# Kernel tuning notes

Measured on AMD Instinct MI355X. Metric: run time of the kernel, lower is better.

Reference implementation:

```python
import jax, jax.numpy as jnp
import numpy as np

DIM = 1024
HEADS = 16
DIM_HEAD = 64
INNER = HEADS * DIM_HEAD  # 1024
SCALE = DIM_HEAD ** -0.5


def setup_inputs() -> dict:
    key = jax.random.key(0)
    k_x, k_qkv, k_ow, k_ob = jax.random.split(key, 4)
    B, N = 4, 2048
    x = jax.random.normal(k_x, (B, N, DIM), dtype=jnp.float32)
    # nn.Linear weights stored as [out, in] in torch; keep [in, out] for x @ W.
    w_qkv = jax.random.normal(k_qkv, (DIM, 3 * INNER), dtype=jnp.float32) * (DIM ** -0.5)
    w_out = jax.random.normal(k_ow, (INNER, DIM), dtype=jnp.float32) * (INNER ** -0.5)
    b_out = jax.random.normal(k_ob, (DIM,), dtype=jnp.float32) * 0.01
    return {"x": x, "w_qkv": w_qkv, "w_out": w_out, "b_out": b_out}


def reference(x, w_qkv, w_out, b_out):
    B, N, _ = x.shape
    qkv = x @ w_qkv  # [B, N, 3*inner]
    q, k, v = jnp.split(qkv, 3, axis=-1)
    # [B, N, inner] -> [B, H, N, dh]
    def to_heads(t):
        return t.reshape(B, N, HEADS, DIM_HEAD).transpose(0, 2, 1, 3)
    q, k, v = to_heads(q), to_heads(k), to_heads(v)
    attn = jnp.einsum("bhqd,bhkd->bhqk", q, k) * SCALE  # [B, H, N, N]
    attn = jax.nn.softmax(attn, axis=-1)
    out = jnp.einsum("bhqk,bhkd->bhqd", attn, v)  # [B, H, N, dh]
    out = out.transpose(0, 2, 1, 3).reshape(B, N, INNER)
    return out @ w_out + b_out
```

## Files before the change

kernel.cpp:

```cpp
#include <hip/hip_runtime.h>
#include <hip/hip_bf16.h>
#include <stdint.h>

typedef __attribute__((ext_vector_type(4))) float f32x4;
typedef __attribute__((ext_vector_type(16))) float f32x16;
typedef __attribute__((ext_vector_type(8))) short s16x8;
typedef __attribute__((ext_vector_type(4))) short s16x4;
typedef __attribute__((ext_vector_type(4))) unsigned int u32x4;

#define DEV static __device__ __forceinline__

constexpr int B_ = 4, H_ = 16, N_ = 2048;
constexpr float CL_ = 0.18033688011112042f;

DEV short f2bf(float x) {
  __hip_bfloat16 h = __float2bfloat16(x);
  return *reinterpret_cast<short*>(&h);
}

DEV uint32_t cvtpk(float lo, float hi) {
  uint32_t r;
  asm("v_cvt_pk_bf16_f32 %0, %1, %2" : "=v"(r) : "v"(lo), "v"(hi));
  return r;
}

DEV void gload16(const void* g, void* l) {
  __builtin_amdgcn_global_load_lds((const __attribute__((address_space(1))) void*)g,
                                   (__attribute__((address_space(3))) void*)l, 16, 0, 0);
}

__global__ void k_cvt(const float* __restrict__ x, short* __restrict__ xb) {
  int i = (blockIdx.x * 256 + threadIdx.x) * 8;
  const float4* p = reinterpret_cast<const float4*>(x + i);
  float4 a = p[0], b = p[1];
  s16x8 o;
  o[0] = f2bf(a.x); o[1] = f2bf(a.y); o[2] = f2bf(a.z); o[3] = f2bf(a.w);
  o[4] = f2bf(b.x); o[5] = f2bf(b.y); o[6] = f2bf(b.z); o[7] = f2bf(b.w);
  *reinterpret_cast<s16x8*>(xb + i) = o;
}

__global__ void k_tw(const float* __restrict__ W, short* __restrict__ WT, int R, int C) {
  __shared__ short t[64][72];
  int r0 = blockIdx.y * 64, c0 = blockIdx.x * 64;
  int tid = threadIdx.x;
  int r = tid >> 2, cp = (tid & 3) * 16;
  const float4* s4 = reinterpret_cast<const float4*>(W + (size_t)(r0 + r) * C + c0 + cp);
  float4 f0 = s4[0], f1 = s4[1], f2 = s4[2], f3 = s4[3];
  short* tr = &t[r][cp];
  tr[0] = f2bf(f0.x); tr[1] = f2bf(f0.y); tr[2]  = f2bf(f0.z); tr[3]  = f2bf(f0.w);
  tr[4] = f2bf(f1.x); tr[5] = f2bf(f1.y); tr[6]  = f2bf(f1.z); tr[7]  = f2bf(f1.w);
  tr[8] = f2bf(f2.x); tr[9] = f2bf(f2.y); tr[10] = f2bf(f2.z); tr[11] = f2bf(f2.w);
  tr[12] = f2bf(f3.x); tr[13] = f2bf(f3.y); tr[14] = f2bf(f3.z); tr[15] = f2bf(f3.w);
  __syncthreads();
  int cc = tid >> 2, rp = (tid & 3) * 16;
  short buf[16];
#pragma unroll
  for (int i = 0; i < 16; ++i) buf[i] = t[rp + i][cc];
  short* dst = WT + (size_t)(c0 + cc) * R + r0 + rp;
  *reinterpret_cast<s16x8*>(dst) = *reinterpret_cast<s16x8*>(buf);
  *reinterpret_cast<s16x8*>(dst + 8) = *reinterpret_cast<s16x8*>(buf + 8);
}

__global__ void k_tv(const short* __restrict__ v, short* __restrict__ vT) {
  __shared__ short t[64][72];
  int bh = blockIdx.y, n0 = blockIdx.x * 64;
  int tid = threadIdx.x;
  int r = tid >> 2, cp = (tid & 3) * 16;
  const short* src = v + ((size_t)bh * N_ + n0 + r) * 64 + cp;
  *reinterpret_cast<s16x8*>(&t[r][cp]) = *reinterpret_cast<const s16x8*>(src);
  *reinterpret_cast<s16x8*>(&t[r][cp + 8]) = *reinterpret_cast<const s16x8*>(src + 8);
  __syncthreads();
  int d = tid >> 2, np = (tid & 3) * 16;
  short buf[16];
#pragma unroll
  for (int i = 0; i < 16; ++i) buf[i] = t[np + i][d];
  short* dst = vT + ((size_t)bh * 64 + d) * N_ + n0 + np;
  *reinterpret_cast<s16x8*>(dst) = *reinterpret_cast<s16x8*>(buf);
  *reinterpret_cast<s16x8*>(dst + 8) = *reinterpret_cast<s16x8*>(buf + 8);
}

template <int EPI>
__global__ __launch_bounds__(256, 2)
void k_gemm(const short* __restrict__ A, const short* __restrict__ BT,
            int M, int N, int K,
            short* __restrict__ oq, short* __restrict__ ok, short* __restrict__ ov,
            const float* __restrict__ bias, float* __restrict__ out) {
  __shared__ short As[128 * 32];
  __shared__ short Bs[128 * 32];
  const int tid = threadIdx.x;
  const int m0 = blockIdx.x * 128, n0 = blockIdx.y * 128;
  const int lane = tid & 63, w = tid >> 6, g = lane >> 4, c = lane & 15;
  const int wr = w >> 1, wc = w & 1;
  f32x4 acc[4][4] = {};
  const int trow = tid >> 2, tk = (tid & 3) * 8;
  const short* ga = A + (size_t)(m0 + trow) * K + tk;
  const short* gb = BT + (size_t)(n0 + trow) * K + tk;
  short* la = As + tid * 8;
  short* lb = Bs + tid * 8;
  for (int k0 = 0; k0 < K; k0 += 32) {
    gload16(ga + k0, la);
    gload16(ga + (size_t)64 * K + k0, la + 2048);
    gload16(gb + k0, lb);
    gload16(gb + (size_t)64 * K + k0, lb + 2048);
    __syncthreads();
    s16x8 af[4], bf[4];
#pragma unroll
    for (int i = 0; i < 4; ++i)
      af[i] = *reinterpret_cast<const s16x8*>(As + (wr * 64 + i * 16 + c) * 32 + g * 8);
#pragma unroll
    for (int j = 0; j < 4; ++j)
      bf[j] = *reinterpret_cast<const s16x8*>(Bs + (wc * 64 + j * 16 + c) * 32 + g * 8);
#pragma unroll
    for (int i = 0; i < 4; ++i)
#pragma unroll
      for (int j = 0; j < 4; ++j)
        acc[i][j] = __builtin_amdgcn_mfma_f32_16x16x32_bf16(af[i], bf[j], acc[i][j], 0, 0, 0);
    __syncthreads();
  }
  if (EPI == 0) {
#pragma unroll
    for (int bj = 0; bj < 4; ++bj) {
      int ncol = n0 + wc * 64 + bj * 16 + c;
      int part = ncol >> 10;
      int c10 = ncol & 1023;
      int h = c10 >> 6, d = c10 & 63;
      short* dst0 = part == 0 ? oq : (part == 1 ? ok : ov);
      float qs = (part == 0) ? CL_ : 1.0f;
#pragma unroll
      for (int ai = 0; ai < 4; ++ai) {
#pragma unroll
        for (int r = 0; r < 4; ++r) {
          int mrow = m0 + wr * 64 + ai * 16 + g * 4 + r;
          int b = mrow >> 11, nr = mrow & 2047;
          dst0[((size_t)((b * H_ + h) * N_ + nr) << 6) + d] = f2bf(acc[ai][bj][r] * qs);
        }
      }
    }
  } else {
#pragma unroll
    for (int bj = 0; bj < 4; ++bj) {
      int ncol = n0 + wc * 64 + bj * 16 + c;
      float bb = bias[ncol];
#pragma unroll
      for (int ai = 0; ai < 4; ++ai) {
#pragma unroll
        for (int r = 0; r < 4; ++r) {
          int mrow = m0 + wr * 64 + ai * 16 + g * 4 + r;
          out[(size_t)mrow * N + ncol] = acc[ai][bj][r] + bb;
        }
      }
    }
  }
}

__global__ __launch_bounds__(256, 2)
void k_attn(const short* __restrict__ q, const short* __restrict__ kk,
            const short* __restrict__ vT, short* __restrict__ ao) {
  __shared__ __align__(16) char smem[65536];
  constexpr int NT = N_ / 64;
  int bh = blockIdx.x, qb = blockIdx.y;
  int b = bh >> 4, head = bh & 15;
  int tid = threadIdx.x, w = tid >> 6, lane = tid & 63;
  int half = lane >> 5, qc = lane & 31;
  const size_t ho = (size_t)bh * (N_ * 64);
  const short* Q = q + ho;
  const char* Kc = reinterpret_cast<const char*>(kk + ho);
  const char* Vc = reinterpret_cast<const char*>(vT + ho);
  int q0w = qb * 256 + w * 64;
  s16x8 qf[2][4];
#pragma unroll
  for (int i = 0; i < 2; ++i)
#pragma unroll
    for (int ks = 0; ks < 4; ++ks)
      qf[i][ks] = *reinterpret_cast<const s16x8*>(Q + (size_t)(q0w + i * 32 + qc) * 64 + ks * 16 + half * 8);
  f32x16 ot[2][2] = {};
  float lp[2] = {0.f, 0.f};
  const int rsw = (qc & 7) << 4;
  const int s_i0 = tid, s_i1 = tid + 256;
  const int s_r0 = s_i0 >> 3, s_c0 = ((s_i0 & 7) << 4) ^ ((s_r0 & 7) << 4);
  const int s_r1 = s_i1 >> 3, s_c1 = ((s_i1 & 7) << 4) ^ ((s_r1 & 7) << 4);
#define STAGE(T)                                                                       \
  {                                                                                    \
    char* nb = smem + ((T) & 3) * 16384;                                               \
    gload16(Kc + (size_t)((T) * 64 + s_r0) * 128 + s_c0, nb + s_i0 * 16);              \
    gload16(Kc + (size_t)((T) * 64 + s_r1) * 128 + s_c1, nb + s_i1 * 16);              \
    gload16(Vc + (size_t)s_r0 * 4096 + (T) * 128 + s_c0, nb + 8192 + s_i0 * 16);       \
    gload16(Vc + (size_t)s_r1 * 4096 + (T) * 128 + s_c1, nb + 8192 + s_i1 * 16);       \
  }
  STAGE(0);
  STAGE(1);
  for (int tt = 0; tt < NT; ++tt) {
    if (tt + 2 < NT) STAGE(tt + 2);
    if (tt + 2 < NT) {
      asm volatile("s_waitcnt vmcnt(8)" ::: "memory");
    } else if (tt + 1 < NT) {
      asm volatile("s_waitcnt vmcnt(4)" ::: "memory");
    } else {
      asm volatile("s_waitcnt vmcnt(0)" ::: "memory");
    }
    __builtin_amdgcn_s_barrier();
    __builtin_amdgcn_sched_barrier(0);
    const char* kb_ = smem + (tt & 3) * 16384;
    const char* vb_ = kb_ + 8192;
    s16x8 kf[2][4];
#pragma unroll
    for (int j = 0; j < 2; ++j)
#pragma unroll
      for (int ks = 0; ks < 4; ++ks)
        kf[j][ks] = *reinterpret_cast<const s16x8*>(kb_ + (j * 32 + qc) * 128 + ((ks * 32 + half * 16) ^ rsw));
    f32x16 st[2][2] = {};
    __builtin_amdgcn_s_setprio(1);
#pragma unroll
    for (int j = 0; j < 2; ++j)
#pragma unroll
      for (int i = 0; i < 2; ++i)
#pragma unroll
        for (int ks = 0; ks < 4; ++ks)
          st[j][i] = __builtin_amdgcn_mfma_f32_32x32x16_bf16(kf[j][ks], qf[i][ks], st[j][i], 0, 0, 0);
    __builtin_amdgcn_s_setprio(0);
#pragma unroll
    for (int j = 0; j < 2; ++j)
#pragma unroll
      for (int i = 0; i < 2; ++i)
#pragma unroll
        for (int r = 0; r < 16; ++r) {
          float p = __builtin_amdgcn_exp2f(st[j][i][r]);
          st[j][i][r] = p;
          lp[i] += p;
        }
    u32x4 pwv[2][4];
#pragma unroll
    for (int j = 0; j < 2; ++j)
#pragma unroll
      for (int i = 0; i < 2; ++i)
#pragma unroll
        for (int bb = 0; bb < 2; ++bb)
#pragma unroll
          for (int p = 0; p < 2; ++p) {
            uint32_t Aw = cvtpk(st[j][i][8 * bb + 2 * p], st[j][i][8 * bb + 2 * p + 1]);
            uint32_t Bw = cvtpk(st[j][i][8 * bb + 4 + 2 * p], st[j][i][8 * bb + 4 + 2 * p + 1]);
            asm volatile("v_permlane32_swap_b32 %0, %1" : "+v"(Aw), "+v"(Bw));
            pwv[i][j * 2 + bb][p] = Aw;
            pwv[i][j * 2 + bb][p + 2] = Bw;
          }
    s16x8 vf[2][4];
#pragma unroll
    for (int db = 0; db < 2; ++db)
#pragma unroll
      for (int kb4 = 0; kb4 < 4; ++kb4)
        vf[db][kb4] = *reinterpret_cast<const s16x8*>(vb_ + (db * 32 + qc) * 128 + ((kb4 * 32 + half * 16) ^ rsw));
    __builtin_amdgcn_s_setprio(1);
#pragma unroll
    for (int db = 0; db < 2; ++db)
#pragma unroll
      for (int i = 0; i < 2; ++i)
#pragma unroll
        for (int kb4 = 0; kb4 < 4; ++kb4)
          ot[db][i] = __builtin_amdgcn_mfma_f32_32x32x16_bf16(
              vf[db][kb4], __builtin_bit_cast(s16x8, pwv[i][kb4]), ot[db][i], 0, 0, 0);
    __builtin_amdgcn_s_setprio(0);
  }
#undef STAGE
  float inv[2];
#pragma unroll
  for (int i = 0; i < 2; ++i) {
    float t = lp[i] + __shfl_xor(lp[i], 32, 64);
    inv[i] = 1.f / t;
  }
  short* Oq = reinterpret_cast<short*>(smem) + w * 2304;
#pragma unroll
  for (int i = 0; i < 2; ++i) {
#pragma unroll
    for (int db = 0; db < 2; ++db)
#pragma unroll
      for (int m = 0; m < 4; ++m) {
        uint2 pk;
        pk.x = cvtpk(ot[db][i][4 * m] * inv[i], ot[db][i][4 * m + 1] * inv[i]);
        pk.y = cvtpk(ot[db][i][4 * m + 2] * inv[i], ot[db][i][4 * m + 3] * inv[i]);
        *reinterpret_cast<uint2*>(Oq + qc * 72 + db * 32 + m * 8 + half * 4) = pk;
      }
    int q2 = lane >> 1, dcol = (lane & 1) * 32;
    size_t ro = (size_t)(b * N_ + q0w + i * 32 + q2) * 1024 + head * 64 + dcol;
#pragma unroll
    for (int ch = 0; ch < 4; ++ch) {
      s16x8 vv = *reinterpret_cast<const s16x8*>(Oq + q2 * 72 + dcol + ch * 8);
      *reinterpret_cast<s16x8*>(ao + ro + ch * 8) = vv;
    }
  }
}

extern "C" void kernel_launch(void* const* d_in, const int* in_sizes, int n_in,
                              void* d_out, int out_size, void* d_ws, size_t ws_size,
                              hipStream_t stream) {
  const float* x = (const float*)d_in[0];
  const float* w_qkv = (const float*)d_in[1];
  const float* w_out = (const float*)d_in[2];
  const float* b_out = (const float*)d_in[3];
  float* out = (float*)d_out;
  char* ws = (char*)d_ws;
  short* xb    = (short*)(ws);
  short* wqkvT = (short*)(ws + 16777216);
  short* woutT = (short*)(ws + 23068672);
  short* qB    = (short*)(ws + 25165824);
  short* kB    = (short*)(ws + 41943040);
  short* vtmp  = (short*)(ws + 58720256);
  short* vTT   = (short*)(ws + 75497472);
  short* ao    = xb;

  k_cvt<<<4096, 256, 0, stream>>>(x, xb);
  k_tw<<<dim3(48, 16), 256, 0, stream>>>(w_qkv, wqkvT, 1024, 3072);
  k_tw<<<dim3(16, 16), 256, 0, stream>>>(w_out, woutT, 1024, 1024);
  k_gemm<0><<<dim3(64, 24), 256, 0, stream>>>(xb, wqkvT, 8192, 3072, 1024,
                                              qB, kB, vtmp, nullptr, nullptr);
  k_tv<<<dim3(32, 64), 256, 0, stream>>>(vtmp, vTT);
  k_attn<<<dim3(64, 8), 256, 0, stream>>>(qB, kB, vTT, ao);
  k_gemm<1><<<dim3(64, 8), 256, 0, stream>>>(ao, woutT, 8192, 1024, 1024,
                                             nullptr, nullptr, nullptr, b_out, out);
}
```

Before: 191.8 us.

## Halve attention query tile per block and double-buffer smem for higher occupancy

The attention kernel now gives each wave 32 query rows instead of 64, which doubles the grid to 1024 blocks. Shared memory drops to 32KB with two K/V stages instead of four, and launch bounds go from 2 to 4 blocks per CU. The explicit vmcnt-based prefetch of two tiles ahead becomes a one-ahead prefetch with __syncthreads at each step. The goal is higher occupancy and fewer registers per thread, at the cost of reloading K/V from global memory twice as often per query and using shallower pipelining.

```diff
diff --git a/kernel.cpp b/kernel.cpp
--- a/kernel.cpp
+++ b/kernel.cpp
@@ -153,10 +153,10 @@
   }
 }
 
-__global__ __launch_bounds__(256, 2)
+__global__ __launch_bounds__(256, 4)
 void k_attn(const short* __restrict__ q, const short* __restrict__ kk,
             const short* __restrict__ vT, short* __restrict__ ao) {
-  __shared__ __align__(16) char smem[65536];
+  __shared__ __align__(16) char smem[32768];
   constexpr int NT = N_ / 64;
   int bh = blockIdx.x, qb = blockIdx.y;
   int b = bh >> 4, head = bh & 15;
@@ -166,126 +166,102 @@
   const short* Q = q + ho;
   const char* Kc = reinterpret_cast<const char*>(kk + ho);
   const char* Vc = reinterpret_cast<const char*>(vT + ho);
-  int q0w = qb * 256 + w * 64;
-  s16x8 qf[2][4];
-#pragma unroll
-  for (int i = 0; i < 2; ++i)
-#pragma unroll
-    for (int ks = 0; ks < 4; ++ks)
-      qf[i][ks] = *reinterpret_cast<const s16x8*>(Q + (size_t)(q0w + i * 32 + qc) * 64 + ks * 16 + half * 8);
-  f32x16 ot[2][2] = {};
-  float lp[2] = {0.f, 0.f};
+  int q0w = qb * 128 + w * 32;
+  s16x8 qf[4];
+#pragma unroll
+  for (int ks = 0; ks < 4; ++ks)
+    qf[ks] = *reinterpret_cast<const s16x8*>(Q + (size_t)(q0w + qc) * 64 + ks * 16 + half * 8);
+  f32x16 ot[2] = {};
+  float lp = 0.f;
   const int rsw = (qc & 7) << 4;
   const int s_i0 = tid, s_i1 = tid + 256;
   const int s_r0 = s_i0 >> 3, s_c0 = ((s_i0 & 7) << 4) ^ ((s_r0 & 7) << 4);
   const int s_r1 = s_i1 >> 3, s_c1 = ((s_i1 & 7) << 4) ^ ((s_r1 & 7) << 4);
 #define STAGE(T)                                                                       \
   {                                                                                    \
-    char* nb = smem + ((T) & 3) * 16384;                                               \
+    char* nb = smem + ((T) & 1) * 16384;                                               \
     gload16(Kc + (size_t)((T) * 64 + s_r0) * 128 + s_c0, nb + s_i0 * 16);              \
     gload16(Kc + (size_t)((T) * 64 + s_r1) * 128 + s_c1, nb + s_i1 * 16);              \
     gload16(Vc + (size_t)s_r0 * 4096 + (T) * 128 + s_c0, nb + 8192 + s_i0 * 16);       \
     gload16(Vc + (size_t)s_r1 * 4096 + (T) * 128 + s_c1, nb + 8192 + s_i1 * 16);       \
   }
   STAGE(0);
-  STAGE(1);
+  __syncthreads();
   for (int tt = 0; tt < NT; ++tt) {
-    if (tt + 2 < NT) STAGE(tt + 2);
-    if (tt + 2 < NT) {
-      asm volatile("s_waitcnt vmcnt(8)" ::: "memory");
-    } else if (tt + 1 < NT) {
-      asm volatile("s_waitcnt vmcnt(4)" ::: "memory");
-    } else {
-      asm volatile("s_waitcnt vmcnt(0)" ::: "memory");
-    }
-    __builtin_amdgcn_s_barrier();
-    __builtin_amdgcn_sched_barrier(0);
-    const char* kb_ = smem + (tt & 3) * 16384;
+    if (tt + 1 < NT) STAGE(tt + 1);
+    const char* kb_ = smem + (tt & 1) * 16384;
     const char* vb_ = kb_ + 8192;
-    s16x8 kf[2][4];
+    f32x16 st[2];
+#pragma unroll
+    for (int j = 0; j < 2; ++j) {
+      s16x8 kfj[4];
+#pragma unroll
+      for (int ks = 0; ks < 4; ++ks)
+        kfj[ks] = *reinterpret_cast<const s16x8*>(kb_ + (j * 32 + qc) * 128 + ((ks * 32 + half * 16) ^ rsw));
+      f32x16 acc = {};
+      __builtin_amdgcn_s_setprio(1);
+#pragma unroll
+      for (int ks = 0; ks < 4; ++ks)
+        acc = __builtin_amdgcn_mfma_f32_32x32x16_bf16(kfj[ks], qf[ks], acc, 0, 0, 0);
+      __builtin_amdgcn_s_setprio(0);
+      st[j] = acc;
+    }
 #pragma unroll
     for (int j = 0; j < 2; ++j)
 #pragma unroll
-      for (int ks = 0; ks < 4; ++ks)
-        kf[j][ks] = *reinterpret_cast<const s16x8*>(kb_ + (j * 32 + qc) * 128 + ((ks * 32 + half * 16) ^ rsw));
-    f32x16 st[2][2] = {};
-    __builtin_amdgcn_s_setprio(1);
+      for (int r = 0; r < 16; ++r) {
+        float p = __builtin_amdgcn_exp2f(st[j][r]);
+        st[j][r] = p;
+        lp += p;
+      }
+    u32x4 pwv[4];
 #pragma unroll
     for (int j = 0; j < 2; ++j)
 #pragma unroll
-      for (int i = 0; i < 2; ++i)
-#pragma unroll
-        for (int ks = 0; ks < 4; ++ks)
-          st[j][i] = __builtin_amdgcn_mfma_f32_32x32x16_bf16(kf[j][ks], qf[i][ks], st[j][i], 0, 0, 0);
-    __builtin_amdgcn_s_setprio(0);
-#pragma unroll
-    for (int j = 0; j < 2; ++j)
-#pragma unroll
-      for (int i = 0; i < 2; ++i)
-#pragma unroll
-        for (int r = 0; r < 16; ++r) {
-          float p = __builtin_amdgcn_exp2f(st[j][i][r]);
-          st[j][i][r] = p;
-          lp[i] += p;
+      for (int bb = 0; bb < 2; ++bb)
+#pragma unroll
+        for (int p = 0; p < 2; ++p) {
+          uint32_t Aw = cvtpk(st[j][8 * bb + 2 * p], st[j][8 * bb + 2 * p + 1]);
+          uint32_t Bw = cvtpk(st[j][8 * bb + 4 + 2 * p], st[j][8 * bb + 4 + 2 * p + 1]);
+          asm volatile("v_permlane32_swap_b32 %0, %1" : "+v"(Aw), "+v"(Bw));
+          pwv[j * 2 + bb][p] = Aw;
+          pwv[j * 2 + bb][p + 2] = Bw;
         }
-    u32x4 pwv[2][4];
-#pragma unroll
-    for (int j = 0; j < 2; ++j)
-#pragma unroll
-      for (int i = 0; i < 2; ++i)
-#pragma unroll
-        for (int bb = 0; bb < 2; ++bb)
-#pragma unroll
-          for (int p = 0; p < 2; ++p) {
-            uint32_t Aw = cvtpk(st[j][i][8 * bb + 2 * p], st[j][i][8 * bb + 2 * p + 1]);
-            uint32_t Bw = cvtpk(st[j][i][8 * bb + 4 + 2 * p], st[j][i][8 * bb + 4 + 2 * p + 1]);
-            asm volatile("v_permlane32_swap_b32 %0, %1" : "+v"(Aw), "+v"(Bw));
-            pwv[i][j * 2 + bb][p] = Aw;
-            pwv[i][j * 2 + bb][p + 2] = Bw;
-          }
-    s16x8 vf[2][4];
-#pragma unroll
-    for (int db = 0; db < 2; ++db)
+#pragma unroll
+    for (int db = 0; db < 2; ++db) {
+      s16x8 vf[4];
 #pragma unroll
       for (int kb4 = 0; kb4 < 4; ++kb4)
-        vf[db][kb4] = *reinterpret_cast<const s16x8*>(vb_ + (db * 32 + qc) * 128 + ((kb4 * 32 + half * 16) ^ rsw));
-    __builtin_amdgcn_s_setprio(1);
-#pragma unroll
-    for (int db = 0; db < 2; ++db)
-#pragma unroll
-      for (int i = 0; i < 2; ++i)
-#pragma unroll
-        for (int kb4 = 0; kb4 < 4; ++kb4)
-          ot[db][i] = __builtin_amdgcn_mfma_f32_32x32x16_bf16(
-              vf[db][kb4], __builtin_bit_cast(s16x8, pwv[i][kb4]), ot[db][i], 0, 0, 0);
-    __builtin_amdgcn_s_setprio(0);
+        vf[kb4] = *reinterpret_cast<const s16x8*>(vb_ + (db * 32 + qc) * 128 + ((kb4 * 32 + half * 16) ^ rsw));
+      f32x16 acc = ot[db];
+      __builtin_amdgcn_s_setprio(1);
+#pragma unroll
+      for (int kb4 = 0; kb4 < 4; ++kb4)
+        acc = __builtin_amdgcn_mfma_f32_32x32x16_bf16(
+            vf[kb4], __builtin_bit_cast(s16x8, pwv[kb4]), acc, 0, 0, 0);
+      __builtin_amdgcn_s_setprio(0);
+      ot[db] = acc;
+    }
+    __syncthreads();
   }
 #undef STAGE
-  float inv[2];
-#pragma unroll
-  for (int i = 0; i < 2; ++i) {
-    float t = lp[i] + __shfl_xor(lp[i], 32, 64);
-    inv[i] = 1.f / t;
-  }
+  float linv = 1.f / (lp + __shfl_xor(lp, 32, 64));
   short* Oq = reinterpret_cast<short*>(smem) + w * 2304;
 #pragma unroll
-  for (int i = 0; i < 2; ++i) {
-#pragma unroll
-    for (int db = 0; db < 2; ++db)
-#pragma unroll
-      for (int m = 0; m < 4; ++m) {
-        uint2 pk;
-        pk.x = cvtpk(ot[db][i][4 * m] * inv[i], ot[db][i][4 * m + 1] * inv[i]);
-        pk.y = cvtpk(ot[db][i][4 * m + 2] * inv[i], ot[db][i][4 * m + 3] * inv[i]);
-        *reinterpret_cast<uint2*>(Oq + qc * 72 + db * 32 + m * 8 + half * 4) = pk;
-      }
-    int q2 = lane >> 1, dcol = (lane & 1) * 32;
-    size_t ro = (size_t)(b * N_ + q0w + i * 32 + q2) * 1024 + head * 64 + dcol;
-#pragma unroll
-    for (int ch = 0; ch < 4; ++ch) {
-      s16x8 vv = *reinterpret_cast<const s16x8*>(Oq + q2 * 72 + dcol + ch * 8);
-      *reinterpret_cast<s16x8*>(ao + ro + ch * 8) = vv;
-    }
+  for (int db = 0; db < 2; ++db)
+#pragma unroll
+    for (int m = 0; m < 4; ++m) {
+      uint2 pk;
+      pk.x = cvtpk(ot[db][4 * m] * linv, ot[db][4 * m + 1] * linv);
+      pk.y = cvtpk(ot[db][4 * m + 2] * linv, ot[db][4 * m + 3] * linv);
+      *reinterpret_cast<uint2*>(Oq + qc * 72 + db * 32 + m * 8 + half * 4) = pk;
+    }
+  int q2 = lane >> 1, dcol = (lane & 1) * 32;
+  size_t ro = (size_t)(b * N_ + q0w + q2) * 1024 + head * 64 + dcol;
+#pragma unroll
+  for (int ch = 0; ch < 4; ++ch) {
+    s16x8 vv = *reinterpret_cast<const s16x8*>(Oq + q2 * 72 + dcol + ch * 8);
+    *reinterpret_cast<s16x8*>(ao + ro + ch * 8) = vv;
   }
 }
 
@@ -313,7 +289,7 @@
   k_gemm<0><<<dim3(64, 24), 256, 0, stream>>>(xb, wqkvT, 8192, 3072, 1024,
                                               qB, kB, vtmp, nullptr, nullptr);
   k_tv<<<dim3(32, 64), 256, 0, stream>>>(vtmp, vTT);
-  k_attn<<<dim3(64, 8), 256, 0, stream>>>(qB, kB, vTT, ao);
+  k_attn<<<dim3(64, 16), 256, 0, stream>>>(qB, kB, vTT, ao);
   k_gemm<1><<<dim3(64, 8), 256, 0, stream>>>(ao, woutT, 8192, 1024, 1024,
                                              nullptr, nullptr, nullptr, b_out, out);
 }
```

After: 198.8 us. 3.6% more time.
